# Optimization experiments

Measured on AMD Instinct MI355X. Metric: run time of the kernel, lower is better.

Reference implementation:

```python
import jax, jax.numpy as jnp
import numpy as np


def _compute_deltas(ts, m):
    """Affine time-decay recurrence: delta_0 = 0; for t>=1:
    delta_t = gap_t + (1 - m_{t-1}) * delta_{t-1}, with gap broadcast over features.
    ts: [b, s] timestamps, m: [b, s, f] float 0/1 mask. Returns [b, s, f]."""
    b, s, f = m.shape
    gaps = ts[:, 1:] - ts[:, :-1]          # [b, s-1]
    a = 1.0 - m[:, :-1, :]                 # [b, s-1, f] decay coefficient

    def step(d, inp):
        g_t, a_t = inp                      # g_t: [b], a_t: [b, f]
        d = g_t[:, None] + a_t * d
        return d, d

    gT = jnp.swapaxes(gaps, 0, 1)          # [s-1, b]
    aT = jnp.swapaxes(a, 0, 1)             # [s-1, b, f]
    _, ds = jax.lax.scan(step, jnp.zeros((b, f), ts.dtype), (gT, aT))
    ds = jnp.swapaxes(ds, 0, 1)            # [b, s-1, f]
    return jnp.concatenate([jnp.zeros((b, 1, f), ts.dtype), ds], axis=1)


def setup_inputs() -> dict:
    key = jax.random.key(0)
    k1, k2, k3 = jax.random.split(key, 3)
    b, s, f = 32, 2048, 768
    # monotonically increasing timestamps (cumsum of positive gaps)
    gaps = jax.random.uniform(k1, (b, s), minval=1.0, maxval=60.0, dtype=jnp.float32)
    timestamps = jnp.cumsum(gaps, axis=1)
    encoded_data = jax.random.normal(k2, (b, s, f), dtype=jnp.float32)
    masks = jax.random.randint(k3, (b, s, f), 0, 2, dtype=jnp.int32)
    return {"timestamps": timestamps, "encoded_data": encoded_data, "masks": masks}


def reference(timestamps, encoded_data, masks):
    """JAX translation of _prepare_brits_data. Returns stacked
    [forward_deltas, backward_deltas, backward_X] of shape [3, b, s, f].
    (forward X / masks are pass-through inputs; backward mask is flip(masks).)"""
    m = masks.astype(timestamps.dtype)
    forward_deltas = _compute_deltas(timestamps, m)
    ts_b = jnp.flip(timestamps, axis=1)
    m_b = jnp.flip(m, axis=1)
    backward_deltas = jnp.abs(_compute_deltas(ts_b, m_b))
    x_b = jnp.flip(encoded_data, axis=1)
    return jnp.stack([forward_deltas, backward_deltas, x_b], axis=0)
```

## Files before the change

### kernel.cpp

```cpp
#include <hip/hip_runtime.h>
#include <stdint.h>

static constexpr int B = 32, S = 2048, F = 768;
static constexpr int SC = 64;
static constexpr int NSC = S / SC;
static constexpr int F4 = F / 4;
static constexpr int FT = F4;

__global__ __launch_bounds__(FT) void fusedK(const float* __restrict__ ts,
                                             const float4* __restrict__ x,
                                             const int4* __restrict__ masks,
                                             float* __restrict__ out) {
    const int blk = blockIdx.x;
    const int b  = blk >> 5;
    const int sc = blk & (NSC - 1);
    const int g0 = sc * SC;
    const int j  = threadIdx.x;
    const float* tsb = ts + (size_t)b * S;
    const int4* mbase = masks + (size_t)b * S * F4 + j;

    __shared__ float tss[SC];
    if (threadIdx.x < SC) tss[threadIdx.x] = tsb[g0 + threadIdx.x];
    __syncthreads();

    float t0v = tsb[0];
    float p0 = t0v, p1 = t0v, p2 = t0v, p3 = t0v;
    if (g0 > 0) {
        unsigned um = 0xFu;
        int r = g0 - 1;
        while (um && r >= 0) {
            int rl = (r - 7 > 0) ? r - 7 : 0;
            int nn = r - rl + 1;
            int4 mv[8];
            #pragma unroll
            for (int q = 0; q < 8; ++q) if (q < nn) mv[q] = mbase[(size_t)(r - q) * F4];
            #pragma unroll
            for (int q = 0; q < 8; ++q) if (q < nn) {
                float t = tsb[r - q];
                if ((um & 1u) && mv[q].x) { p0 = t; um &= ~1u; }
                if ((um & 2u) && mv[q].y) { p1 = t; um &= ~2u; }
                if ((um & 4u) && mv[q].z) { p2 = t; um &= ~4u; }
                if ((um & 8u) && mv[q].w) { p3 = t; um &= ~8u; }
            }
            r = rl - 1;
        }
    }

    float tev = tsb[S - 1];
    float n0 = tev, n1 = tev, n2 = tev, n3 = tev;
    if (g0 + SC < S) {
        unsigned um = 0xFu;
        int r = g0 + SC;
        while (um && r < S) {
            int rh = (r + 7 < S - 1) ? r + 7 : S - 1;
            int nn = rh - r + 1;
            int4 mv[8];
            #pragma unroll
            for (int q = 0; q < 8; ++q) if (q < nn) mv[q] = mbase[(size_t)(r + q) * F4];
            #pragma unroll
            for (int q = 0; q < 8; ++q) if (q < nn) {
                float t = tsb[r + q];
                if ((um & 1u) && mv[q].x) { n0 = t; um &= ~1u; }
                if ((um & 2u) && mv[q].y) { n1 = t; um &= ~2u; }
                if ((um & 4u) && mv[q].z) { n2 = t; um &= ~4u; }
                if ((um & 8u) && mv[q].w) { n3 = t; um &= ~8u; }
            }
            r = rh + 1;
        }
    }

    const size_t N4 = (size_t)B * S * F4;
    float4* o0 = reinterpret_cast<float4*>(out) + (size_t)(b * S + g0) * F4 + j;
    float4* o1b = reinterpret_cast<float4*>(out) + N4 + (size_t)b * S * F4 + j;
    float4* o2 = reinterpret_cast<float4*>(out) + 2 * N4 + (size_t)(b * S + g0) * F4 + j;
    const float4* xb = x + (size_t)b * S * F4 + j;

    uint32_t a0 = 0, a1 = 0, a2 = 0, a3 = 0;
    #pragma unroll
    for (int k = 0; k < 32; ++k) {
        int4 mv = mbase[(size_t)(g0 + k) * F4];
        float t = tss[k];
        o0[(size_t)k * F4] = make_float4(t - p0, t - p1, t - p2, t - p3);
        uint32_t bit = 1u << k;
        if (mv.x) { a0 |= bit; p0 = t; }
        if (mv.y) { a1 |= bit; p1 = t; }
        if (mv.z) { a2 |= bit; p2 = t; }
        if (mv.w) { a3 |= bit; p3 = t; }
    }
    uint32_t c0 = 0, c1 = 0, c2 = 0, c3 = 0;
    #pragma unroll
    for (int k = 32; k < 64; ++k) {
        int4 mv = mbase[(size_t)(g0 + k) * F4];
        float t = tss[k];
        o0[(size_t)k * F4] = make_float4(t - p0, t - p1, t - p2, t - p3);
        uint32_t bit = 1u << (k - 32);
        if (mv.x) { c0 |= bit; p0 = t; }
        if (mv.y) { c1 |= bit; p1 = t; }
        if (mv.z) { c2 |= bit; p2 = t; }
        if (mv.w) { c3 |= bit; p3 = t; }
    }

    #pragma unroll
    for (int k = 63; k >= 32; --k) {
        float t = tss[k];
        size_t fr = (size_t)(S - 1 - g0 - k) * F4;
        float4 xv = xb[fr];
        o1b[fr] = make_float4(n0 - t, n1 - t, n2 - t, n3 - t);
        o2[(size_t)k * F4] = xv;
        uint32_t bit = 1u << (k - 32);
        if (c0 & bit) n0 = t;
        if (c1 & bit) n1 = t;
        if (c2 & bit) n2 = t;
        if (c3 & bit) n3 = t;
    }
    #pragma unroll
    for (int k = 31; k >= 0; --k) {
        float t = tss[k];
        size_t fr = (size_t)(S - 1 - g0 - k) * F4;
        float4 xv = xb[fr];
        o1b[fr] = make_float4(n0 - t, n1 - t, n2 - t, n3 - t);
        o2[(size_t)k * F4] = xv;
        uint32_t bit = 1u << k;
        if (a0 & bit) n0 = t;
        if (a1 & bit) n1 = t;
        if (a2 & bit) n2 = t;
        if (a3 & bit) n3 = t;
    }
}

extern "C" void kernel_launch(void* const* d_in, const int* in_sizes, int n_in,
                              void* d_out, int out_size, void* d_ws, size_t ws_size,
                              hipStream_t stream) {
    const float* ts    = (const float*)d_in[0];
    const float4* x    = (const float4*)d_in[1];
    const int4*  masks = (const int4*)d_in[2];
    float* out = (float*)d_out;
    fusedK<<<B * NSC, FT, 0, stream>>>(ts, x, masks, out);
}
```

Before: 238.2 us.

## Split flip-copy into separate blocks and batch mask loads up front

```diff
diff --git a/kernel.cpp b/kernel.cpp
--- a/kernel.cpp
+++ b/kernel.cpp
@@ -12,16 +12,54 @@
                                              const int4* __restrict__ masks,
                                              float* __restrict__ out) {
     const int blk = blockIdx.x;
-    const int b  = blk >> 5;
-    const int sc = blk & (NSC - 1);
+    const int pair = blk >> 1;
+    const int b  = pair >> 5;
+    const int sc = pair & (NSC - 1);
     const int g0 = sc * SC;
     const int j  = threadIdx.x;
+    const size_t N4 = (size_t)B * S * F4;
+
+    if (blk & 1) {
+        const float4* xb = x + (size_t)b * S * F4 + j;
+        float4* o2 = reinterpret_cast<float4*>(out) + 2 * N4 + (size_t)(b * S + g0) * F4 + j;
+        #pragma unroll 8
+        for (int k = 0; k < SC; ++k) {
+            o2[(size_t)k * F4] = xb[(size_t)(S - 1 - g0 - k) * F4];
+        }
+        return;
+    }
+
     const float* tsb = ts + (size_t)b * S;
     const int4* mbase = masks + (size_t)b * S * F4 + j;
 
     __shared__ float tss[SC];
-    if (threadIdx.x < SC) tss[threadIdx.x] = tsb[g0 + threadIdx.x];
+    if (j < SC) tss[j] = tsb[g0 + j];
     __syncthreads();
+
+    uint32_t a0 = 0, a1 = 0, a2 = 0, a3 = 0;
+    uint32_t c0 = 0, c1 = 0, c2 = 0, c3 = 0;
+    #pragma unroll
+    for (int g = 0; g < 8; ++g) {
+        int4 mv[8];
+        #pragma unroll
+        for (int q = 0; q < 8; ++q) mv[q] = mbase[(size_t)(g0 + g * 8 + q) * F4];
+        #pragma unroll
+        for (int q = 0; q < 8; ++q) {
+            const int k = g * 8 + q;
+            const uint32_t bit = 1u << (k & 31);
+            if (k < 32) {
+                if (mv[q].x) a0 |= bit;
+                if (mv[q].y) a1 |= bit;
+                if (mv[q].z) a2 |= bit;
+                if (mv[q].w) a3 |= bit;
+            } else {
+                if (mv[q].x) c0 |= bit;
+                if (mv[q].y) c1 |= bit;
+                if (mv[q].z) c2 |= bit;
+                if (mv[q].w) c3 |= bit;
+            }
+        }
+    }
 
     float t0v = tsb[0];
     float p0 = t0v, p1 = t0v, p2 = t0v, p3 = t0v;
@@ -69,45 +107,35 @@
         }
     }
 
-    const size_t N4 = (size_t)B * S * F4;
     float4* o0 = reinterpret_cast<float4*>(out) + (size_t)(b * S + g0) * F4 + j;
-    float4* o1b = reinterpret_cast<float4*>(out) + N4 + (size_t)b * S * F4 + j;
-    float4* o2 = reinterpret_cast<float4*>(out) + 2 * N4 + (size_t)(b * S + g0) * F4 + j;
-    const float4* xb = x + (size_t)b * S * F4 + j;
-
-    uint32_t a0 = 0, a1 = 0, a2 = 0, a3 = 0;
     #pragma unroll
     for (int k = 0; k < 32; ++k) {
-        int4 mv = mbase[(size_t)(g0 + k) * F4];
         float t = tss[k];
         o0[(size_t)k * F4] = make_float4(t - p0, t - p1, t - p2, t - p3);
-        uint32_t bit = 1u << k;
-        if (mv.x) { a0 |= bit; p0 = t; }
-        if (mv.y) { a1 |= bit; p1 = t; }
-        if (mv.z) { a2 |= bit; p2 = t; }
-        if (mv.w) { a3 |= bit; p3 = t; }
+        const uint32_t bit = 1u << k;
+        if (a0 & bit) p0 = t;
+        if (a1 & bit) p1 = t;
+        if (a2 & bit) p2 = t;
+        if (a3 & bit) p3 = t;
     }
-    uint32_t c0 = 0, c1 = 0, c2 = 0, c3 = 0;
     #pragma unroll
     for (int k = 32; k < 64; ++k) {
-        int4 mv = mbase[(size_t)(g0 + k) * F4];
         float t = tss[k];
         o0[(size_t)k * F4] = make_float4(t - p0, t - p1, t - p2, t - p3);
-        uint32_t bit = 1u << (k - 32);
-        if (mv.x) { c0 |= bit; p0 = t; }
-        if (mv.y) { c1 |= bit; p1 = t; }
-        if (mv.z) { c2 |= bit; p2 = t; }
-        if (mv.w) { c3 |= bit; p3 = t; }
+        const uint32_t bit = 1u << (k - 32);
+        if (c0 & bit) p0 = t;
+        if (c1 & bit) p1 = t;
+        if (c2 & bit) p2 = t;
+        if (c3 & bit) p3 = t;
     }
 
+    float4* o1b = reinterpret_cast<float4*>(out) + N4 + (size_t)b * S * F4 + j;
     #pragma unroll
     for (int k = 63; k >= 32; --k) {
         float t = tss[k];
         size_t fr = (size_t)(S - 1 - g0 - k) * F4;
-        float4 xv = xb[fr];
         o1b[fr] = make_float4(n0 - t, n1 - t, n2 - t, n3 - t);
-        o2[(size_t)k * F4] = xv;
-        uint32_t bit = 1u << (k - 32);
+        const uint32_t bit = 1u << (k - 32);
         if (c0 & bit) n0 = t;
         if (c1 & bit) n1 = t;
         if (c2 & bit) n2 = t;
@@ -117,10 +145,8 @@
     for (int k = 31; k >= 0; --k) {
         float t = tss[k];
         size_t fr = (size_t)(S - 1 - g0 - k) * F4;
-        float4 xv = xb[fr];
         o1b[fr] = make_float4(n0 - t, n1 - t, n2 - t, n3 - t);
-        o2[(size_t)k * F4] = xv;
-        uint32_t bit = 1u << k;
+        const uint32_t bit = 1u << k;
         if (a0 & bit) n0 = t;
         if (a1 & bit) n1 = t;
         if (a2 & bit) n2 = t;
@@ -135,5 +161,5 @@
     const float4* x    = (const float4*)d_in[1];
     const int4*  masks = (const int4*)d_in[2];
     float* out = (float*)d_out;
-    fusedK<<<B * NSC, FT, 0, stream>>>(ts, x, masks, out);
+    fusedK<<<2 * B * NSC, FT, 0, stream>>>(ts, x, masks, out);
 }
```

Measured after the change: 238.0 us. About the same (-0.1%).
